# Performance work log

Measured on AMD Instinct MI355X. Metric: run time of the kernel, lower is better.

## Reference

```python
import jax, jax.numpy as jnp
import numpy as np

B, T, K = 512, 2048, 32


def setup_inputs() -> dict:
    key = jax.random.key(0)
    k1, k2 = jax.random.split(key)
    inputs = jax.random.normal(k1, (B, T, K), dtype=jnp.float32)
    # glorot_uniform for [K, K]
    limit = np.sqrt(6.0 / (K + K)).astype(np.float32)
    transitions = jax.random.uniform(k2, (K, K), dtype=jnp.float32,
                                     minval=-limit, maxval=limit)
    return {"inputs": inputs, "transitions": transitions}


def _crf_decode(potentials, transitions):
    """Viterbi max-sum decode. potentials: [B,T,K], transitions: [K,K].
    Returns (tags [B,T] int32, best_score [B])."""
    first = potentials[:, 0]                      # [B,K]
    rest = jnp.swapaxes(potentials[:, 1:], 0, 1)  # [T-1,B,K]

    def fwd_step(state, pot_t):
        # scores[b, i, j] = state[b, i] + transitions[i, j]
        scores = state[:, :, None] + transitions[None]  # [B,K,K]
        bp = jnp.argmax(scores, axis=1).astype(jnp.int32)  # [B,K] best prev tag
        new_state = jnp.max(scores, axis=1) + pot_t
        return new_state, bp

    final_state, bps = jax.lax.scan(fwd_step, first, rest)  # bps: [T-1,B,K]
    last_tag = jnp.argmax(final_state, axis=-1).astype(jnp.int32)  # [B]
    best_score = jnp.max(final_state, axis=-1)

    def back_step(tag, bp_t):
        prev = jnp.take_along_axis(bp_t, tag[:, None], axis=1)[:, 0]  # [B]
        return prev, prev

    # reverse scan: ys[t] = tag at time t, for t in [0, T-2]
    _, tags_head = jax.lax.scan(back_step, last_tag, bps, reverse=True)
    tags = jnp.concatenate([tags_head, last_tag[None]], axis=0)  # [T,B]
    return jnp.swapaxes(tags, 0, 1), best_score


def reference(inputs, transitions):
    # inference path of CRF.call: viterbi decode -> one_hot
    tags, _ = _crf_decode(inputs, transitions)
    return jax.nn.one_hot(tags, K, dtype=inputs.dtype)  # [B,T,K]
```

## Files before the change

kernel.cpp:

```cpp
#include <hip/hip_runtime.h>

#define CRF_B 512
#define CRF_T 2048
#define CRF_K 32
#define CRF_Q (CRF_T / 4)


__device__ __forceinline__ void crf_step(
    float& vstate, unsigned int& bpack, int sx,
    const float (&trp)[16], const unsigned int (&bpos)[16],
    int hphase, int xmask, float curv)
{
    float val[16];
    val[0] = vstate + trp[0];
#define CRF_GA(m) { int _rb = __builtin_amdgcn_update_dpp(0, __float_as_int(vstate), 0x120 + (m), 0xF, 0xF, false); \
                    val[m] = __int_as_float(_rb) + trp[m]; }
    CRF_GA(1) CRF_GA(2) CRF_GA(3) CRF_GA(4) CRF_GA(5) CRF_GA(6) CRF_GA(7)
    CRF_GA(8) CRF_GA(9) CRF_GA(10) CRF_GA(11) CRF_GA(12) CRF_GA(13) CRF_GA(14) CRF_GA(15)
#undef CRF_GA
    float t8[8];
#pragma unroll
    for (int k = 0; k < 8; ++k) t8[k] = fmaxf(val[k], val[k + 8]);
    float t4[4];
#pragma unroll
    for (int k = 0; k < 4; ++k) t4[k] = fmaxf(t8[k], t8[k + 4]);
    float vmax = fmaxf(fmaxf(t4[0], t4[2]), fmaxf(t4[1], t4[3]));
    unsigned int bm = 0u;
#pragma unroll
    for (int m = 0; m < 16; ++m) bm |= (val[m] == vmax) ? bpos[m] : 0u;
    int myi = (__clz((int)bm) - 16) + (hphase << 4);

    float pv = __shfl_xor(vmax, xmask, 64);
    int   pi = __shfl_xor(myi, xmask, 64);
    bool take = hphase ? (pv >= vmax) : (pv > vmax);
    float w  = take ? pv : vmax;
    int   wi = take ? pi : myi;
    bpack |= ((unsigned int)wi) << (8 * sx);
    vstate = w + curv;
}

__global__ __launch_bounds__(64, 1) void crf_fused(
    const float* __restrict__ pot,
    const float* __restrict__ trans,
    float* __restrict__ out,
    unsigned int* __restrict__ bp)
{
    const int b = blockIdx.x;
    const int l = threadIdx.x;
    const int c = l & 15;
    const int r = l >> 4;
    const int aA = ((r >> 1) << 4) | c;
    const int aB = ((r & 1) << 4) | c;
    const int jA = aB;
    const int hA = r >> 1;
    const int hB = r & 1;

    int idxA[16], idxB[16];
    idxA[0] = aA; idxB[0] = aB;
#define CRF_IDX(m) \
    idxA[m] = __builtin_amdgcn_update_dpp(0, aA, 0x120 + (m), 0xF, 0xF, false); \
    idxB[m] = __builtin_amdgcn_update_dpp(0, aB, 0x120 + (m), 0xF, 0xF, false);
    CRF_IDX(1) CRF_IDX(2) CRF_IDX(3) CRF_IDX(4) CRF_IDX(5) CRF_IDX(6) CRF_IDX(7)
    CRF_IDX(8) CRF_IDX(9) CRF_IDX(10) CRF_IDX(11) CRF_IDX(12) CRF_IDX(13) CRF_IDX(14) CRF_IDX(15)
#undef CRF_IDX

    float trA[16], trB[16];
    unsigned int bpos[16];
#pragma unroll
    for (int m = 0; m < 16; ++m) {
        trA[m]  = trans[idxA[m] * CRF_K + aB];
        trB[m]  = trans[idxB[m] * CRF_K + aA];
        bpos[m] = 1u << (15 - (idxA[m] & 15));
    }

    const float* potb = pot + (size_t)b * (CRF_T * CRF_K);
    unsigned int* bpb = bp + (size_t)b * (CRF_Q * CRF_K);
    float* outb = out + (size_t)b * (CRF_T * CRF_K);

    const int aoff[4] = { aA, aB, aA, aB };

    float vstate = potb[aA];

    float cur[4], nxt[4], nx2[4];
    cur[0] = 0.0f;
#pragma unroll
    for (int t = 1; t < 4; ++t) cur[t] = potb[t * CRF_K + aoff[t]];
#pragma unroll
    for (int sx = 0; sx < 4; ++sx) nxt[sx] = potb[(4 + sx) * CRF_K + aoff[sx]];

    for (int q = 0; q < CRF_Q; ++q) {
        {
            const int tb = (q + 2) * 4;
#pragma unroll
            for (int sx = 0; sx < 4; ++sx) {
                int t = tb + sx; if (t > CRF_T - 1) t = CRF_T - 1;
                nx2[sx] = potb[t * CRF_K + aoff[sx]];
            }
        }
        unsigned int bpack = 0;
        if (q)  crf_step(vstate, bpack, 0, trB, bpos, hB, 16, cur[0]);
        crf_step(vstate, bpack, 1, trA, bpos, hA, 32, cur[1]);
        crf_step(vstate, bpack, 2, trB, bpos, hB, 16, cur[2]);
        crf_step(vstate, bpack, 3, trA, bpos, hA, 32, cur[3]);
        if (r == 0 || r == 3) bpb[q * CRF_K + jA] = bpack;
#pragma unroll
        for (int sx = 0; sx < 4; ++sx) { cur[sx] = nxt[sx]; nxt[sx] = nx2[sx]; }
    }

    __shared__ float fs[CRF_K];
    fs[aB] = vstate;
    __syncthreads();
    int bt = 0; float bv = fs[0];
#pragma unroll
    for (int jj = 1; jj < CRF_K; ++jj) {
        float v = fs[jj];
        if (v > bv) { bv = v; bt = jj; }
    }
    int stag = __builtin_amdgcn_readfirstlane(bt);

    const int col = l & 31;
    outb[(CRF_T - 1) * CRF_K + col] = (col == stag) ? 1.0f : 0.0f;

    __threadfence();

    for (int q0 = CRF_Q - 16; q0 >= 0; q0 -= 16) {
        unsigned int colv[16];
#pragma unroll
        for (int rr = 0; rr < 16; ++rr) colv[rr] = bpb[(q0 + rr) * CRF_K + col];
#pragma unroll
        for (int rr = 15; rr >= 0; --rr) {
#pragma unroll
            for (int bi = 3; bi >= 0; --bi) {
                const int t = (q0 + rr) * 4 + bi;
                if (t == 0) continue;
                unsigned int dw = (unsigned int)__builtin_amdgcn_readlane((int)colv[rr], stag);
                stag = (int)((dw >> (8 * bi)) & 255u);
                outb[(size_t)(t - 1) * CRF_K + col] = (col == stag) ? 1.0f : 0.0f;
            }
        }
    }
}

extern "C" void kernel_launch(void* const* d_in, const int* in_sizes, int n_in,
                              void* d_out, int out_size, void* d_ws, size_t ws_size,
                              hipStream_t stream) {
    const float* pot   = (const float*)d_in[0];
    const float* trans = (const float*)d_in[1];
    float* out = (float*)d_out;
    unsigned int* bp = (unsigned int*)d_ws;

    crf_fused<<<dim3(CRF_B), dim3(64), 0, stream>>>(pot, trans, out, bp);
}
```

Before: 820.9 us.

## Split Viterbi into forward-state, parallel backpointer, and backtrace kernels

The fused kernel is split into three launches. The forward pass now keeps only the max-sum state per step, writes it into the output buffer as scratch, and skips the argmax bookkeeping on its serial critical path. A second kernel with 32 blocks per batch recomputes the backpointers in parallel from the stored states, and a third runs the backtrace and overwrites the output with one-hot tags. The shorter serial chain and the wider parallelism come at the cost of extra global traffic for the full state tensor and two additional launches.

```diff
diff --git a/kernel.cpp b/kernel.cpp
--- a/kernel.cpp
+++ b/kernel.cpp
@@ -6,44 +6,54 @@
 #define CRF_Q (CRF_T / 4)
 
 
-__device__ __forceinline__ void crf_step(
-    float& vstate, unsigned int& bpack, int sx,
-    const float (&trp)[16], const unsigned int (&bpos)[16],
-    int hphase, int xmask, float curv)
-{
-    float val[16];
-    val[0] = vstate + trp[0];
-#define CRF_GA(m) { int _rb = __builtin_amdgcn_update_dpp(0, __float_as_int(vstate), 0x120 + (m), 0xF, 0xF, false); \
-                    val[m] = __int_as_float(_rb) + trp[m]; }
-    CRF_GA(1) CRF_GA(2) CRF_GA(3) CRF_GA(4) CRF_GA(5) CRF_GA(6) CRF_GA(7)
-    CRF_GA(8) CRF_GA(9) CRF_GA(10) CRF_GA(11) CRF_GA(12) CRF_GA(13) CRF_GA(14) CRF_GA(15)
-#undef CRF_GA
-    float t8[8];
-#pragma unroll
-    for (int k = 0; k < 8; ++k) t8[k] = fmaxf(val[k], val[k + 8]);
-    float t4[4];
-#pragma unroll
-    for (int k = 0; k < 4; ++k) t4[k] = fmaxf(t8[k], t8[k + 4]);
-    float vmax = fmaxf(fmaxf(t4[0], t4[2]), fmaxf(t4[1], t4[3]));
-    unsigned int bm = 0u;
-#pragma unroll
-    for (int m = 0; m < 16; ++m) bm |= (val[m] == vmax) ? bpos[m] : 0u;
-    int myi = (__clz((int)bm) - 16) + (hphase << 4);
-
-    float pv = __shfl_xor(vmax, xmask, 64);
-    int   pi = __shfl_xor(myi, xmask, 64);
-    bool take = hphase ? (pv >= vmax) : (pv > vmax);
-    float w  = take ? pv : vmax;
-    int   wi = take ? pi : myi;
-    bpack |= ((unsigned int)wi) << (8 * sx);
-    vstate = w + curv;
-}
-
-__global__ __launch_bounds__(64, 1) void crf_fused(
+
+#define CRF_GATHER16(vsrc, trp, val)                                              \
+    val[0] = (vsrc) + trp[0];                                                     \
+    { int _rb;                                                                    \
+      _rb = __builtin_amdgcn_update_dpp(0, __float_as_int(vsrc), 0x121, 0xF, 0xF, false); val[1]  = __int_as_float(_rb) + trp[1];  \
+      _rb = __builtin_amdgcn_update_dpp(0, __float_as_int(vsrc), 0x122, 0xF, 0xF, false); val[2]  = __int_as_float(_rb) + trp[2];  \
+      _rb = __builtin_amdgcn_update_dpp(0, __float_as_int(vsrc), 0x123, 0xF, 0xF, false); val[3]  = __int_as_float(_rb) + trp[3];  \
+      _rb = __builtin_amdgcn_update_dpp(0, __float_as_int(vsrc), 0x124, 0xF, 0xF, false); val[4]  = __int_as_float(_rb) + trp[4];  \
+      _rb = __builtin_amdgcn_update_dpp(0, __float_as_int(vsrc), 0x125, 0xF, 0xF, false); val[5]  = __int_as_float(_rb) + trp[5];  \
+      _rb = __builtin_amdgcn_update_dpp(0, __float_as_int(vsrc), 0x126, 0xF, 0xF, false); val[6]  = __int_as_float(_rb) + trp[6];  \
+      _rb = __builtin_amdgcn_update_dpp(0, __float_as_int(vsrc), 0x127, 0xF, 0xF, false); val[7]  = __int_as_float(_rb) + trp[7];  \
+      _rb = __builtin_amdgcn_update_dpp(0, __float_as_int(vsrc), 0x128, 0xF, 0xF, false); val[8]  = __int_as_float(_rb) + trp[8];  \
+      _rb = __builtin_amdgcn_update_dpp(0, __float_as_int(vsrc), 0x129, 0xF, 0xF, false); val[9]  = __int_as_float(_rb) + trp[9];  \
+      _rb = __builtin_amdgcn_update_dpp(0, __float_as_int(vsrc), 0x12A, 0xF, 0xF, false); val[10] = __int_as_float(_rb) + trp[10]; \
+      _rb = __builtin_amdgcn_update_dpp(0, __float_as_int(vsrc), 0x12B, 0xF, 0xF, false); val[11] = __int_as_float(_rb) + trp[11]; \
+      _rb = __builtin_amdgcn_update_dpp(0, __float_as_int(vsrc), 0x12C, 0xF, 0xF, false); val[12] = __int_as_float(_rb) + trp[12]; \
+      _rb = __builtin_amdgcn_update_dpp(0, __float_as_int(vsrc), 0x12D, 0xF, 0xF, false); val[13] = __int_as_float(_rb) + trp[13]; \
+      _rb = __builtin_amdgcn_update_dpp(0, __float_as_int(vsrc), 0x12E, 0xF, 0xF, false); val[14] = __int_as_float(_rb) + trp[14]; \
+      _rb = __builtin_amdgcn_update_dpp(0, __float_as_int(vsrc), 0x12F, 0xF, 0xF, false); val[15] = __int_as_float(_rb) + trp[15]; }
+
+#define CRF_MAXTREE(val, vmax)                                                    \
+    { float _t8[8], _t4[4];                                                       \
+      _Pragma("unroll") for (int _k = 0; _k < 8; ++_k) _t8[_k] = fmaxf(val[_k], val[_k + 8]); \
+      _Pragma("unroll") for (int _k = 0; _k < 4; ++_k) _t4[_k] = fmaxf(_t8[_k], _t8[_k + 4]); \
+      vmax = fmaxf(fmaxf(_t4[0], _t4[2]), fmaxf(_t4[1], _t4[3])); }
+
+#define CRF_IDXTAB(seed, idx)                                                     \
+    idx[0] = (seed);                                                              \
+    idx[1]  = __builtin_amdgcn_update_dpp(0, (seed), 0x121, 0xF, 0xF, false);     \
+    idx[2]  = __builtin_amdgcn_update_dpp(0, (seed), 0x122, 0xF, 0xF, false);     \
+    idx[3]  = __builtin_amdgcn_update_dpp(0, (seed), 0x123, 0xF, 0xF, false);     \
+    idx[4]  = __builtin_amdgcn_update_dpp(0, (seed), 0x124, 0xF, 0xF, false);     \
+    idx[5]  = __builtin_amdgcn_update_dpp(0, (seed), 0x125, 0xF, 0xF, false);     \
+    idx[6]  = __builtin_amdgcn_update_dpp(0, (seed), 0x126, 0xF, 0xF, false);     \
+    idx[7]  = __builtin_amdgcn_update_dpp(0, (seed), 0x127, 0xF, 0xF, false);     \
+    idx[8]  = __builtin_amdgcn_update_dpp(0, (seed), 0x128, 0xF, 0xF, false);     \
+    idx[9]  = __builtin_amdgcn_update_dpp(0, (seed), 0x129, 0xF, 0xF, false);     \
+    idx[10] = __builtin_amdgcn_update_dpp(0, (seed), 0x12A, 0xF, 0xF, false);     \
+    idx[11] = __builtin_amdgcn_update_dpp(0, (seed), 0x12B, 0xF, 0xF, false);     \
+    idx[12] = __builtin_amdgcn_update_dpp(0, (seed), 0x12C, 0xF, 0xF, false);     \
+    idx[13] = __builtin_amdgcn_update_dpp(0, (seed), 0x12D, 0xF, 0xF, false);     \
+    idx[14] = __builtin_amdgcn_update_dpp(0, (seed), 0x12E, 0xF, 0xF, false);     \
+    idx[15] = __builtin_amdgcn_update_dpp(0, (seed), 0x12F, 0xF, 0xF, false);
+
+__global__ __launch_bounds__(64, 1) void crf_fwd(
     const float* __restrict__ pot,
     const float* __restrict__ trans,
-    float* __restrict__ out,
-    unsigned int* __restrict__ bp)
+    float* __restrict__ st)
 {
     const int b = blockIdx.x;
     const int l = threadIdx.x;
@@ -51,42 +61,33 @@
     const int r = l >> 4;
     const int aA = ((r >> 1) << 4) | c;
     const int aB = ((r & 1) << 4) | c;
-    const int jA = aB;
-    const int hA = r >> 1;
-    const int hB = r & 1;
 
     int idxA[16], idxB[16];
-    idxA[0] = aA; idxB[0] = aB;
-#define CRF_IDX(m) \
-    idxA[m] = __builtin_amdgcn_update_dpp(0, aA, 0x120 + (m), 0xF, 0xF, false); \
-    idxB[m] = __builtin_amdgcn_update_dpp(0, aB, 0x120 + (m), 0xF, 0xF, false);
-    CRF_IDX(1) CRF_IDX(2) CRF_IDX(3) CRF_IDX(4) CRF_IDX(5) CRF_IDX(6) CRF_IDX(7)
-    CRF_IDX(8) CRF_IDX(9) CRF_IDX(10) CRF_IDX(11) CRF_IDX(12) CRF_IDX(13) CRF_IDX(14) CRF_IDX(15)
-#undef CRF_IDX
+    CRF_IDXTAB(aA, idxA)
+    CRF_IDXTAB(aB, idxB)
 
     float trA[16], trB[16];
-    unsigned int bpos[16];
 #pragma unroll
     for (int m = 0; m < 16; ++m) {
-        trA[m]  = trans[idxA[m] * CRF_K + aB];
-        trB[m]  = trans[idxB[m] * CRF_K + aA];
-        bpos[m] = 1u << (15 - (idxA[m] & 15));
-    }
+        trA[m] = trans[idxA[m] * CRF_K + aB];
+        trB[m] = trans[idxB[m] * CRF_K + aA];
+    }
+
+    auto pr = __builtin_amdgcn_permlane32_swap((unsigned)l, (unsigned)l, false, false);
+    const bool use0 = ((int)pr[0] == (l ^ 32));
 
     const float* potb = pot + (size_t)b * (CRF_T * CRF_K);
-    unsigned int* bpb = bp + (size_t)b * (CRF_Q * CRF_K);
-    float* outb = out + (size_t)b * (CRF_T * CRF_K);
-
-    const int aoff[4] = { aA, aB, aA, aB };
+    float* stb = st + (size_t)b * (CRF_T * CRF_K);
 
     float vstate = potb[aA];
+    stb[aA] = vstate;
 
     float cur[4], nxt[4], nx2[4];
     cur[0] = 0.0f;
 #pragma unroll
-    for (int t = 1; t < 4; ++t) cur[t] = potb[t * CRF_K + aoff[t]];
-#pragma unroll
-    for (int sx = 0; sx < 4; ++sx) nxt[sx] = potb[(4 + sx) * CRF_K + aoff[sx]];
+    for (int t = 1; t < 4; ++t) cur[t] = potb[t * CRF_K + ((t & 1) ? aB : aA)];
+#pragma unroll
+    for (int sx = 0; sx < 4; ++sx) nxt[sx] = potb[(4 + sx) * CRF_K + ((sx & 1) ? aB : aA)];
 
     for (int q = 0; q < CRF_Q; ++q) {
         {
@@ -94,21 +95,122 @@
 #pragma unroll
             for (int sx = 0; sx < 4; ++sx) {
                 int t = tb + sx; if (t > CRF_T - 1) t = CRF_T - 1;
-                nx2[sx] = potb[t * CRF_K + aoff[sx]];
+                nx2[sx] = potb[t * CRF_K + ((sx & 1) ? aB : aA)];
             }
         }
-        unsigned int bpack = 0;
-        if (q)  crf_step(vstate, bpack, 0, trB, bpos, hB, 16, cur[0]);
-        crf_step(vstate, bpack, 1, trA, bpos, hA, 32, cur[1]);
-        crf_step(vstate, bpack, 2, trB, bpos, hB, 16, cur[2]);
-        crf_step(vstate, bpack, 3, trA, bpos, hA, 32, cur[3]);
-        if (r == 0 || r == 3) bpb[q * CRF_K + jA] = bpack;
+        if (q) {
+            float val[16], vmax;
+            CRF_GATHER16(vstate, trB, val)
+            CRF_MAXTREE(val, vmax)
+            float pv = __int_as_float(__builtin_amdgcn_ds_swizzle(__float_as_int(vmax), 0x401F));
+            vstate = fmaxf(vmax, pv) + cur[0];
+            stb[(4 * q) * CRF_K + aA] = vstate;
+        }
+        {
+            float val[16], vmax;
+            CRF_GATHER16(vstate, trA, val)
+            CRF_MAXTREE(val, vmax)
+            auto sw = __builtin_amdgcn_permlane32_swap(__float_as_uint(vmax), __float_as_uint(vmax), false, false);
+            float pv = __uint_as_float(use0 ? (unsigned)sw[0] : (unsigned)sw[1]);
+            vstate = fmaxf(vmax, pv) + cur[1];
+            stb[(4 * q + 1) * CRF_K + aB] = vstate;
+        }
+        {
+            float val[16], vmax;
+            CRF_GATHER16(vstate, trB, val)
+            CRF_MAXTREE(val, vmax)
+            float pv = __int_as_float(__builtin_amdgcn_ds_swizzle(__float_as_int(vmax), 0x401F));
+            vstate = fmaxf(vmax, pv) + cur[2];
+            stb[(4 * q + 2) * CRF_K + aA] = vstate;
+        }
+        {
+            float val[16], vmax;
+            CRF_GATHER16(vstate, trA, val)
+            CRF_MAXTREE(val, vmax)
+            auto sw = __builtin_amdgcn_permlane32_swap(__float_as_uint(vmax), __float_as_uint(vmax), false, false);
+            float pv = __uint_as_float(use0 ? (unsigned)sw[0] : (unsigned)sw[1]);
+            vstate = fmaxf(vmax, pv) + cur[3];
+            stb[(4 * q + 3) * CRF_K + aB] = vstate;
+        }
 #pragma unroll
         for (int sx = 0; sx < 4; ++sx) { cur[sx] = nxt[sx]; nxt[sx] = nx2[sx]; }
     }
-
+}
+
+__global__ __launch_bounds__(64, 1) void crf_bpk(
+    const float* __restrict__ st,
+    const float* __restrict__ trans,
+    unsigned int* __restrict__ bp)
+{
+    const int blk = blockIdx.x;
+    const int b = blk >> 5;
+    const int k = blk & 31;
+    const int l = threadIdx.x;
+    const int c = l & 15;
+    const int r = l >> 4;
+    const int h = r & 1;
+    const int aB = (h << 4) | c;
+    const int j = ((r >> 1) << 4) | c;
+
+    int idxB[16];
+    CRF_IDXTAB(aB, idxB)
+    float trB[16]; unsigned int bpos[16];
+#pragma unroll
+    for (int m = 0; m < 16; ++m) {
+        trB[m]  = trans[idxB[m] * CRF_K + j];
+        bpos[m] = 1u << (15 - (idxB[m] & 15));
+    }
+
+    const float* stb = st + (size_t)b * (CRF_T * CRF_K);
+    unsigned int* bpb = bp + (size_t)b * (CRF_Q * CRF_K);
+
+    const int q0 = k * 16;
+    const int t_first = (q0 == 0) ? 1 : 4 * q0;
+    float snext = stb[(t_first - 1) * CRF_K + aB];
+
+    for (int q = q0; q < q0 + 16; ++q) {
+        unsigned int dword = 0;
+#pragma unroll
+        for (int sx = 0; sx < 4; ++sx) {
+            const int t = 4 * q + sx;
+            if (q == 0 && sx == 0) continue;
+            float s = snext;
+            {
+                int tn = t + 1; if (tn > CRF_T - 1) tn = CRF_T - 1;
+                snext = stb[(tn - 1) * CRF_K + aB];
+            }
+            float val[16], vmax;
+            CRF_GATHER16(s, trB, val)
+            CRF_MAXTREE(val, vmax)
+            unsigned int bm = 0u;
+#pragma unroll
+            for (int m = 0; m < 16; ++m) bm |= (val[m] == vmax) ? bpos[m] : 0u;
+            unsigned int idx4 = (unsigned int)(__clz((int)bm) - 16);
+            float pv = __int_as_float(__builtin_amdgcn_ds_swizzle(__float_as_int(vmax), 0x401F));
+            bool W = h ? (vmax > pv) : (pv > vmax);
+            bool own_won = (W == (h != 0));
+            unsigned int byte = own_won ? (idx4 | ((unsigned)h << 4)) : 0u;
+            dword |= byte << (8 * sx);
+        }
+        dword |= (unsigned int)__builtin_amdgcn_ds_swizzle((int)dword, 0x401F);
+        bpb[q * CRF_K + j] = dword;
+    }
+}
+
+__global__ __launch_bounds__(64, 1) void crf_bt(
+    const unsigned int* __restrict__ bp,
+    float* out)
+{
+    const int b = blockIdx.x;
+    const int l = threadIdx.x;
+    const int col = l & 31;
+
+    float* outb = out + (size_t)b * (CRF_T * CRF_K);
+    const unsigned int* bpb = bp + (size_t)b * (CRF_Q * CRF_K);
+
+    float fv = outb[(CRF_T - 1) * CRF_K + col];
     __shared__ float fs[CRF_K];
-    fs[aB] = vstate;
+    fs[col] = fv;
     __syncthreads();
     int bt = 0; float bv = fs[0];
 #pragma unroll
@@ -118,10 +220,7 @@
     }
     int stag = __builtin_amdgcn_readfirstlane(bt);
 
-    const int col = l & 31;
     outb[(CRF_T - 1) * CRF_K + col] = (col == stag) ? 1.0f : 0.0f;
-
-    __threadfence();
 
     for (int q0 = CRF_Q - 16; q0 >= 0; q0 -= 16) {
         unsigned int colv[16];
@@ -149,5 +248,7 @@
     float* out = (float*)d_out;
     unsigned int* bp = (unsigned int*)d_ws;
 
-    crf_fused<<<dim3(CRF_B), dim3(64), 0, stream>>>(pot, trans, out, bp);
-}
+    crf_fwd<<<dim3(CRF_B),      dim3(64), 0, stream>>>(pot, trans, out);
+    crf_bpk<<<dim3(CRF_B * 32), dim3(64), 0, stream>>>(out, trans, bp);
+    crf_bt <<<dim3(CRF_B),      dim3(64), 0, stream>>>(bp, out);
+}
```

Result: faster. 665.8 us (-18.9%).
